# Kernel optimization log

Hardware: AMD Instinct MI355X
Metric: run time of the kernel (lower is better)

## Reference

```python
import jax, jax.numpy as jnp
import numpy as np
from jax import lax

B, C, H, W = 4096, 3, 32, 32
IN_FEATURE = C * H * W  # 3072
CLAMP = 0.7  # cifar10 axonLimit bounds


def _spike(v):
    # threshold.forward (cifar10): max(0, sign(v))  -> heaviside, sign(0)=0
    return jnp.where(v > 0, 1.0, 0.0).astype(v.dtype)


def setup_inputs() -> dict:
    key = jax.random.key(0)
    ks = jax.random.split(key, 6)
    x = jax.random.normal(ks[0], (B, IN_FEATURE, 4), dtype=jnp.float32)
    tau_m1 = jax.random.uniform(ks[1], (IN_FEATURE,), dtype=jnp.float32)
    tau_s1 = jax.random.uniform(ks[2], (IN_FEATURE,), dtype=jnp.float32)
    tau_sm1 = jax.random.uniform(ks[3], (IN_FEATURE,), dtype=jnp.float32)
    gauss_kernel = jax.random.normal(ks[4], (C, C, 3, 3), dtype=jnp.float32) * 0.1
    gauss_bias = jnp.zeros((C,), dtype=jnp.float32)
    return {
        "x": x,
        "tau_m1": tau_m1,
        "tau_s1": tau_s1,
        "tau_sm1": tau_sm1,
        "gauss_kernel": gauss_kernel,
        "gauss_bias": gauss_bias,
        "weight": 1,
    }


def reference(x, tau_m1, tau_s1, tau_sm1, gauss_kernel, gauss_bias, weight):
    # point_cul_Layer.forward, cifar10, activation indices fixed to (elu, negative, leakyrelu)
    x1, x2, x3, reset = x[..., 0], x[..., 1], x[..., 2], x[..., 3]
    y = (jax.nn.elu(x1) * tau_m1
         + (-x2) * tau_s1
         + jnp.where(x3 >= 0, x3, 0.01 * x3) * tau_sm1)  # [B, IN_FEATURE]
    # STuning: subtract heaviside spike of reset scaled by 2**weight
    y = y - _spike(reset) / (2.0 ** weight)
    # weight_rand: learnable 3x3 'gaussian' conv over the image view (B,3,32,32)
    img = y.reshape(B, C, H, W)
    m = lax.conv_general_dilated(
        img, gauss_kernel, window_strides=(1, 1), padding="SAME",
        dimension_numbers=("NCHW", "OIHW", "NCHW"))
    m = m + gauss_bias[None, :, None, None]
    y = m.reshape(B, IN_FEATURE)
    # axonLimit (cifar10): clamp to [-0.7, 0.7]
    return jnp.clip(y, -CLAMP, CLAMP)
```

## Files before the change

kernel.cpp:

```cpp
#include <hip/hip_runtime.h>
#include <math.h>

#define BLK 256
#define CH 3
#define INF 3072
#define PH 34
#define PW 36

__device__ __forceinline__ float pointwise(float4 v, float tm, float ts, float tsm,
                                           float inv2w) {
    const float el = (v.x > 0.f) ? v.x : expm1f(v.x);
    const float lr = (v.z >= 0.f) ? v.z : 0.01f * v.z;
    float r = el * tm;
    r = fmaf(-v.y, ts, r);
    r = fmaf(lr, tsm, r);
    return (v.w > 0.f) ? r - inv2w : r;
}

__global__ __launch_bounds__(BLK) void fused_point_conv_kernel(
    const float4* __restrict__ x,
    const float4* __restrict__ tm4,
    const float4* __restrict__ ts4,
    const float4* __restrict__ tsm4,
    const float* __restrict__ gk,
    const float* __restrict__ gb,
    const int*  __restrict__ weight,
    float4* __restrict__ out)
{
    __shared__ float y[CH][PH][PW];
    __shared__ float sk[CH * CH * 9];
    __shared__ float sb[CH];

    const int b = blockIdx.x;
    const int t = threadIdx.x;

    for (int i = t; i < CH * 200; i += BLK) {
        const int c = i / 200;
        const int r = i - c * 200;
        int row, col;
        if (r < 36)      { row = 0;  col = r; }
        else if (r < 72) { row = 33; col = r - 36; }
        else { const int rr = r - 72; row = 1 + (rr >> 2);
               const int sel = rr & 3; col = (sel == 0) ? 0 : 32 + sel; }
        y[c][row][col] = 0.f;
    }
    if (t < CH * CH * 9) sk[t] = gk[t];
    if (t < CH) sb[t] = gb[t];

    const float inv2w = exp2f(-(float)weight[0]);
    const int h  = t >> 3;
    const int w0 = (t & 7) << 2;
    const size_t xbase = (size_t)b * INF;

    __syncthreads();

    #pragma unroll
    for (int j = 0; j < 3; ++j) {
        const int f0 = (j << 10) + (t << 2);
        const float4 v0 = x[xbase + f0 + 0];
        const float4 v1 = x[xbase + f0 + 1];
        const float4 v2 = x[xbase + f0 + 2];
        const float4 v3 = x[xbase + f0 + 3];
        const int q = (j << 8) + t;
        const float4 tm = tm4[q], ts = ts4[q], tsm = tsm4[q];
        float* yrow = &y[j][h + 1][w0 + 1];
        yrow[0] = pointwise(v0, tm.x, ts.x, tsm.x, inv2w);
        yrow[1] = pointwise(v1, tm.y, ts.y, tsm.y, inv2w);
        yrow[2] = pointwise(v2, tm.z, ts.z, tsm.z, inv2w);
        yrow[3] = pointwise(v3, tm.w, ts.w, tsm.w, inv2w);
    }
    __syncthreads();

    #pragma unroll
    for (int j = 0; j < 3; ++j) {
        const float bias = sb[j];
        float a0 = bias, a1 = bias, a2 = bias, a3 = bias;
        #pragma unroll
        for (int ci = 0; ci < CH; ++ci) {
            #pragma unroll
            for (int kh = 0; kh < 3; ++kh) {
                const float4 s4 = *(const float4*)&y[ci][h + kh][w0];
                const float2 s2 = *(const float2*)&y[ci][h + kh][w0 + 4];
                const int kb = ((j * CH + ci) * 3 + kh) * 3;
                const float k0 = sk[kb + 0], k1 = sk[kb + 1], k2 = sk[kb + 2];
                a0 = fmaf(s4.x, k0, a0); a0 = fmaf(s4.y, k1, a0); a0 = fmaf(s4.z, k2, a0);
                a1 = fmaf(s4.y, k0, a1); a1 = fmaf(s4.z, k1, a1); a1 = fmaf(s4.w, k2, a1);
                a2 = fmaf(s4.z, k0, a2); a2 = fmaf(s4.w, k1, a2); a2 = fmaf(s2.x, k2, a2);
                a3 = fmaf(s4.w, k0, a3); a3 = fmaf(s2.x, k1, a3); a3 = fmaf(s2.y, k2, a3);
            }
        }
        a0 = fminf(fmaxf(a0, -0.7f), 0.7f);
        a1 = fminf(fmaxf(a1, -0.7f), 0.7f);
        a2 = fminf(fmaxf(a2, -0.7f), 0.7f);
        a3 = fminf(fmaxf(a3, -0.7f), 0.7f);
        out[(size_t)b * (INF / 4) + (j << 8) + t] = make_float4(a0, a1, a2, a3);
    }
}

extern "C" void kernel_launch(void* const* d_in, const int* in_sizes, int n_in,
                              void* d_out, int out_size, void* d_ws, size_t ws_size,
                              hipStream_t stream) {
    const float4* x    = (const float4*)d_in[0];
    const float4* tm4  = (const float4*)d_in[1];
    const float4* ts4  = (const float4*)d_in[2];
    const float4* tsm4 = (const float4*)d_in[3];
    const float*  gk   = (const float*)d_in[4];
    const float*  gb   = (const float*)d_in[5];
    const int*    wgt  = (const int*)d_in[6];
    float4* out = (float4*)d_out;

    const int B = in_sizes[0] / (INF * 4);
    fused_point_conv_kernel<<<B, BLK, 0, stream>>>(
        x, tm4, ts4, tsm4, gk, gb, wgt, out);
}
```

Before: 49.56 us.

## Process four images per block with double-buffered LDS and register prefetch

```diff
diff --git a/kernel.cpp b/kernel.cpp
--- a/kernel.cpp
+++ b/kernel.cpp
@@ -6,6 +6,7 @@
 #define INF 3072
 #define PH 34
 #define PW 36
+#define IMGS 4
 
 __device__ __forceinline__ float pointwise(float4 v, float tm, float ts, float tsm,
                                            float inv2w) {
@@ -19,97 +20,112 @@
 
 __global__ __launch_bounds__(BLK) void fused_point_conv_kernel(
     const float4* __restrict__ x,
-    const float4* __restrict__ tm4,
-    const float4* __restrict__ ts4,
-    const float4* __restrict__ tsm4,
+    const float* __restrict__ tau_m1,
+    const float* __restrict__ tau_s1,
+    const float* __restrict__ tau_sm1,
     const float* __restrict__ gk,
     const float* __restrict__ gb,
     const int*  __restrict__ weight,
     float4* __restrict__ out)
 {
-    __shared__ float y[CH][PH][PW];
-    __shared__ float sk[CH * CH * 9];
+    __shared__ __align__(16) float y[2][CH][PH][PW];
+    __shared__ float sk[81];
     __shared__ float sb[CH];
 
-    const int b = blockIdx.x;
     const int t = threadIdx.x;
+    const int b0 = blockIdx.x * IMGS;
 
-    for (int i = t; i < CH * 200; i += BLK) {
-        const int c = i / 200;
-        const int r = i - c * 200;
+    for (int i = t; i < 2 * CH * 200; i += BLK) {
+        const int buf = i / 600;
+        const int rem = i - buf * 600;
+        const int c = rem / 200;
+        const int r = rem - c * 200;
         int row, col;
         if (r < 36)      { row = 0;  col = r; }
         else if (r < 72) { row = 33; col = r - 36; }
         else { const int rr = r - 72; row = 1 + (rr >> 2);
                const int sel = rr & 3; col = (sel == 0) ? 0 : 32 + sel; }
-        y[c][row][col] = 0.f;
+        y[buf][c][row][col] = 0.f;
     }
-    if (t < CH * CH * 9) sk[t] = gk[t];
+    if (t < 81) sk[t] = gk[t];
     if (t < CH) sb[t] = gb[t];
 
     const float inv2w = exp2f(-(float)weight[0]);
     const int h  = t >> 3;
     const int w0 = (t & 7) << 2;
-    const size_t xbase = (size_t)b * INF;
 
-    __syncthreads();
+    float4 vx[12];
+    {
+        const size_t base = (size_t)b0 * INF + t;
+        #pragma unroll
+        for (int i = 0; i < 12; ++i) vx[i] = x[base + (i << 8)];
+    }
 
-    #pragma unroll
-    for (int j = 0; j < 3; ++j) {
-        const int f0 = (j << 10) + (t << 2);
-        const float4 v0 = x[xbase + f0 + 0];
-        const float4 v1 = x[xbase + f0 + 1];
-        const float4 v2 = x[xbase + f0 + 2];
-        const float4 v3 = x[xbase + f0 + 3];
-        const int q = (j << 8) + t;
-        const float4 tm = tm4[q], ts = ts4[q], tsm = tsm4[q];
-        float* yrow = &y[j][h + 1][w0 + 1];
-        yrow[0] = pointwise(v0, tm.x, ts.x, tsm.x, inv2w);
-        yrow[1] = pointwise(v1, tm.y, ts.y, tsm.y, inv2w);
-        yrow[2] = pointwise(v2, tm.z, ts.z, tsm.z, inv2w);
-        yrow[3] = pointwise(v3, tm.w, ts.w, tsm.w, inv2w);
-    }
-    __syncthreads();
+    for (int k = 0; k < IMGS; ++k) {
+        const int b = b0 + k;
 
-    #pragma unroll
-    for (int j = 0; j < 3; ++j) {
-        const float bias = sb[j];
-        float a0 = bias, a1 = bias, a2 = bias, a3 = bias;
+        float* ybuf = &y[k & 1][0][0][0];
         #pragma unroll
-        for (int ci = 0; ci < CH; ++ci) {
+        for (int i = 0; i < 12; ++i) {
+            const int f = (i << 8) + t;
+            const float tm  = tau_m1[f];
+            const float ts  = tau_s1[f];
+            const float tsm = tau_sm1[f];
+            const int c = f >> 10, hw = f & 1023;
+            const int hh = hw >> 5, ww = hw & 31;
+            ybuf[(c * PH + hh + 1) * PW + ww + 1] =
+                pointwise(vx[i], tm, ts, tsm, inv2w);
+        }
+
+        if (k + 1 < IMGS) {
+            const size_t base = (size_t)(b + 1) * INF + t;
             #pragma unroll
-            for (int kh = 0; kh < 3; ++kh) {
-                const float4 s4 = *(const float4*)&y[ci][h + kh][w0];
-                const float2 s2 = *(const float2*)&y[ci][h + kh][w0 + 4];
-                const int kb = ((j * CH + ci) * 3 + kh) * 3;
-                const float k0 = sk[kb + 0], k1 = sk[kb + 1], k2 = sk[kb + 2];
-                a0 = fmaf(s4.x, k0, a0); a0 = fmaf(s4.y, k1, a0); a0 = fmaf(s4.z, k2, a0);
-                a1 = fmaf(s4.y, k0, a1); a1 = fmaf(s4.z, k1, a1); a1 = fmaf(s4.w, k2, a1);
-                a2 = fmaf(s4.z, k0, a2); a2 = fmaf(s4.w, k1, a2); a2 = fmaf(s2.x, k2, a2);
-                a3 = fmaf(s4.w, k0, a3); a3 = fmaf(s2.x, k1, a3); a3 = fmaf(s2.y, k2, a3);
+            for (int i = 0; i < 12; ++i) vx[i] = x[base + (i << 8)];
+        }
+
+        __syncthreads();
+
+        const float (*yc)[PH][PW] = y[k & 1];
+        #pragma unroll
+        for (int j = 0; j < CH; ++j) {
+            const float bias = sb[j];
+            float a0 = bias, a1 = bias, a2 = bias, a3 = bias;
+            #pragma unroll
+            for (int ci = 0; ci < CH; ++ci) {
+                #pragma unroll
+                for (int kh = 0; kh < 3; ++kh) {
+                    const float4 s4 = *(const float4*)&yc[ci][h + kh][w0];
+                    const float2 s2 = *(const float2*)&yc[ci][h + kh][w0 + 4];
+                    const int kb = ((j * CH + ci) * 3 + kh) * 3;
+                    const float k0 = sk[kb + 0], k1 = sk[kb + 1], k2 = sk[kb + 2];
+                    a0 = fmaf(s4.x, k0, a0); a0 = fmaf(s4.y, k1, a0); a0 = fmaf(s4.z, k2, a0);
+                    a1 = fmaf(s4.y, k0, a1); a1 = fmaf(s4.z, k1, a1); a1 = fmaf(s4.w, k2, a1);
+                    a2 = fmaf(s4.z, k0, a2); a2 = fmaf(s4.w, k1, a2); a2 = fmaf(s2.x, k2, a2);
+                    a3 = fmaf(s4.w, k0, a3); a3 = fmaf(s2.x, k1, a3); a3 = fmaf(s2.y, k2, a3);
+                }
             }
+            a0 = fminf(fmaxf(a0, -0.7f), 0.7f);
+            a1 = fminf(fmaxf(a1, -0.7f), 0.7f);
+            a2 = fminf(fmaxf(a2, -0.7f), 0.7f);
+            a3 = fminf(fmaxf(a3, -0.7f), 0.7f);
+            out[(size_t)b * (INF / 4) + (j << 8) + t] = make_float4(a0, a1, a2, a3);
         }
-        a0 = fminf(fmaxf(a0, -0.7f), 0.7f);
-        a1 = fminf(fmaxf(a1, -0.7f), 0.7f);
-        a2 = fminf(fmaxf(a2, -0.7f), 0.7f);
-        a3 = fminf(fmaxf(a3, -0.7f), 0.7f);
-        out[(size_t)b * (INF / 4) + (j << 8) + t] = make_float4(a0, a1, a2, a3);
     }
 }
 
 extern "C" void kernel_launch(void* const* d_in, const int* in_sizes, int n_in,
                               void* d_out, int out_size, void* d_ws, size_t ws_size,
                               hipStream_t stream) {
-    const float4* x    = (const float4*)d_in[0];
-    const float4* tm4  = (const float4*)d_in[1];
-    const float4* ts4  = (const float4*)d_in[2];
-    const float4* tsm4 = (const float4*)d_in[3];
-    const float*  gk   = (const float*)d_in[4];
-    const float*  gb   = (const float*)d_in[5];
-    const int*    wgt  = (const int*)d_in[6];
+    const float4* x      = (const float4*)d_in[0];
+    const float* tau_m1  = (const float*)d_in[1];
+    const float* tau_s1  = (const float*)d_in[2];
+    const float* tau_sm1 = (const float*)d_in[3];
+    const float* gk      = (const float*)d_in[4];
+    const float* gb      = (const float*)d_in[5];
+    const int*   wgt     = (const int*)d_in[6];
     float4* out = (float4*)d_out;
 
     const int B = in_sizes[0] / (INF * 4);
-    fused_point_conv_kernel<<<B, BLK, 0, stream>>>(
-        x, tm4, ts4, tsm4, gk, gb, wgt, out);
+    fused_point_conv_kernel<<<B / IMGS, BLK, 0, stream>>>(
+        x, tau_m1, tau_s1, tau_sm1, gk, gb, wgt, out);
 }
```

After: 77.98 us. 1.57x slower.
